# Performance work log

Hardware: AMD Instinct MI355X
Metric: run time of the kernel (lower is better)

The kernel has to match this reference:

```python
import jax, jax.numpy as jnp
import numpy as np

V, N, D, H, C = 3, 4096, 512, 128, 5  # views, nodes, in_dim, hidden, classes
NEG = -9.0e15   # mask value from original code (-9000000000000000.0)
NEG_SLOPE = 0.25


def _leaky(x, slope):
    return jnp.where(x >= 0, x, slope * x)


def setup_inputs() -> dict:
    key = jax.random.key(0)
    ks = jax.random.split(key, 24)
    g = lambda i, shape, s=0.05: (jax.random.normal(ks[i], shape, dtype=jnp.float32) * s)
    return {
        "data": jax.random.normal(ks[0], (V, N, D), dtype=jnp.float32),
        "adj": jax.random.randint(ks[1], (V, N, N), 0, 2, dtype=jnp.int32),
        "gac_w": g(2, (V, D, H)), "gac_b": g(3, (V, H)),
        "a1": g(4, (V, H)), "a2": g(5, (V, H)),
        "mlp_w": g(6, (V, D, H)), "mlp_b": g(7, (V, H)),
        "q_w": g(8, (V, H, H)), "q_b": g(9, (V, H)),
        "k_w": g(10, (V, H, H)), "k_b": g(11, (V, H)),
        "v_w": g(12, (V, H, H)), "v_b": g(13, (V, H)),
        "fc_w": g(14, (V, H, H)), "fc_b": g(15, (V, H)),
        "conf_w": g(16, (V, H, 1)), "conf_b": g(17, (V, 1)),
        "mm_w": g(18, (V * H, C)), "mm_b": g(19, (C,)),
    }


def reference(data, adj, gac_w, gac_b, a1, a2, mlp_w, mlp_b,
              q_w, q_b, k_w, k_b, v_w, v_b, fc_w, fc_b,
              conf_w, conf_b, mm_w, mm_b):
    # --- GraphAttentionConv (per view, vectorized over v) ---
    h = jnp.einsum('vnd,vdh->vnh', data, gac_w)               # spmm(input, W)
    e1 = jnp.einsum('vnh,vh->vn', h, a1)                      # h @ a1
    e2 = jnp.einsum('vnh,vh->vn', h, a2)                      # h @ a2
    e = _leaky(e1[:, :, None] + e2[:, None, :], NEG_SLOPE)    # [V,N,N] broadcast-add
    e = jnp.where(adj > 0, e, NEG)                            # mask by dense adjacency
    att = jax.nn.softmax(e, axis=-1)                          # row softmax
    feat = jnp.einsum('vnm,vmh->vnh', att, h) + gac_b[:, None, :]
    feat = _leaky(feat, NEG_SLOPE)                            # F.leaky_relu(GAC out, 0.25)
    # residual MLP branch
    feat = feat + jnp.einsum('vnd,vdh->vnh', data, mlp_w) + mlp_b[:, None, :]

    # --- StructureGuidedFeatureEnhancement (n_heads=1): per-node HxH attention ---
    Q = jnp.einsum('vnh,vho->vno', feat, q_w) + q_b[:, None, :]
    K = jnp.einsum('vnh,vho->vno', feat, k_w) + k_b[:, None, :]
    Vv = jnp.einsum('vnh,vho->vno', feat, v_w) + v_b[:, None, :]
    scale = jnp.sqrt(jnp.asarray(H, jnp.float32))
    A = Q[:, :, :, None] * K[:, :, None, :] / scale           # [V,N,H,H] outer product
    A = jax.nn.softmax(A, axis=-1)
    agg = jnp.einsum('vnio,vno->vni', A, Vv)                  # attention @ V
    agg = jnp.einsum('vnh,vho->vno', agg, fc_w) + fc_b[:, None, :]
    feat = jax.nn.relu(agg)

    # --- TCP confidence gating ---
    conf = jnp.einsum('vnh,vho->vno', feat, conf_w) + conf_b[:, None, :]  # [V,N,1]
    feat = feat * conf

    # --- concat views along feature dim, final classifier ---
    mm = jnp.transpose(feat, (1, 0, 2)).reshape(N, V * H)     # [N, V*H]
    return mm @ mm_w + mm_b                                   # MMlogit [N, C]
```

## Files before the change

kernel.cpp:

```cpp
#include <hip/hip_runtime.h>
#include <hip/hip_bf16.h>

#define V 3
#define N 4096
#define D 512
#define H 128
#define C 5
#define KS 4
#define M2 64
#define M1 32
#define LOG2E 1.4426950408889634f

typedef short short8 __attribute__((ext_vector_type(8)));
typedef float floatx4 __attribute__((ext_vector_type(4)));
typedef int   intx4  __attribute__((ext_vector_type(4)));

__device__ __forceinline__ unsigned short f2bf(float f){
  __hip_bfloat16 h = __float2bfloat16(f);
  return *reinterpret_cast<unsigned short*>(&h);
}
__device__ __forceinline__ unsigned int pk_bf16(float a, float b){
  unsigned int ua = __float_as_uint(a), ub = __float_as_uint(b);
  ua += 0x7FFFu + ((ua >> 16) & 1u);
  ub += 0x7FFFu + ((ub >> 16) & 1u);
  return (ua >> 16) | (ub & 0xFFFF0000u);
}

__global__ __launch_bounds__(256) void k0_wt(
    const float* __restrict__ gw, const float* __restrict__ mw,
    unsigned short* __restrict__ wT)
{
  const int v = blockIdx.x, m = blockIdx.y, kc = blockIdx.z;
  const int t = threadIdx.x;
  __shared__ unsigned short tr[128*72];
  const float* src = (m ? mw : gw) + (size_t)v*D*H + (size_t)kc*64*H;
  for (int i = t; i < 64*128; i += 256){
    int kk = i >> 7, col = i & 127;
    tr[col*72 + kk] = f2bf(src[i]);
  }
  __syncthreads();
  const int col = t >> 1, half = t & 1;
  uint4* dst = (uint4*)(wT + (((size_t)m*V + v)*H + col)*D + kc*64 + half*32);
  const unsigned short* s = &tr[col*72 + half*32];
  dst[0] = *(const uint4*)(s);
  dst[1] = *(const uint4*)(s + 8);
  dst[2] = *(const uint4*)(s + 16);
  dst[3] = *(const uint4*)(s + 24);
}

__global__ __launch_bounds__(256) void k0b_wt(
    const float* __restrict__ qw, const float* __restrict__ kw,
    const float* __restrict__ vw, const float* __restrict__ fw,
    unsigned short* __restrict__ wq4T)
{
  const int v = blockIdx.x, m = blockIdx.y, kc = blockIdx.z;
  const int t = threadIdx.x;
  __shared__ unsigned short tr[128*72];
  const float* src = (m==0?qw: m==1?kw: m==2?vw: fw) + (size_t)v*H*H + (size_t)kc*64*H;
  for (int i = t; i < 64*128; i += 256){
    int kk = i >> 7, col = i & 127;
    tr[col*72 + kk] = f2bf(src[i]);
  }
  __syncthreads();
  const int col = t >> 1, half = t & 1;
  uint4* dst = (uint4*)(wq4T + (((size_t)m*V + v)*H + col)*H + kc*64 + half*32);
  const unsigned short* s = &tr[col*72 + half*32];
  dst[0] = *(const uint4*)(s);
  dst[1] = *(const uint4*)(s + 8);
  dst[2] = *(const uint4*)(s + 16);
  dst[3] = *(const uint4*)(s + 24);
}

__global__ __launch_bounds__(512) void k1_gemm(
    const float* __restrict__ data, const unsigned short* __restrict__ wT,
    const float* __restrict__ a1, const float* __restrict__ a2,
    unsigned short* __restrict__ hT, float* __restrict__ mlp_out,
    float* __restrict__ e1g, float* __restrict__ e2g)
{
  const int v = blockIdx.y;
  const int n0 = blockIdx.x * M1;
  const int t = threadIdx.x;
  const int w = t >> 6, l = t & 63;
  __shared__ __align__(16) unsigned short AT[2][16][64][8];
  __shared__ float epart[2][M1][4];
  unsigned short* hTile = &AT[0][0][0][0];

  {
    const int r = t >> 4, oct = t & 15;
    const float4* dp = (const float4*)(data + ((size_t)v*N + n0 + r)*D + oct*32);
    float4 f[8];
    #pragma unroll
    for (int i=0;i<8;i++) f[i] = dp[i];
    #pragma unroll
    for (int q=0;q<4;q++){
      uint4 u;
      u.x = pk_bf16(f[2*q].x,   f[2*q].y);
      u.y = pk_bf16(f[2*q].z,   f[2*q].w);
      u.z = pk_bf16(f[2*q+1].x, f[2*q+1].y);
      u.w = pk_bf16(f[2*q+1].z, f[2*q+1].w);
      *(uint4*)&AT[r>>4][oct][(r&15) + 16*q][0] = u;
    }
  }
  __syncthreads();
  const int m = w >> 2, cb = (w & 3)*32;
  const int quad = l >> 4, c16 = l & 15;
  const unsigned short* b0 = wT + (((size_t)m*V + v)*H + cb + c16)*D + quad*8;
  floatx4 acc[2][2];
  #pragma unroll
  for (int rt=0;rt<2;rt++) for (int c=0;c<2;c++) acc[rt][c] = (floatx4){0.f,0.f,0.f,0.f};
  #pragma unroll
  for (int ks=0; ks<16; ks++){
    short8 a0 = *(const short8*)&AT[0][ks][l][0];
    short8 a1f = *(const short8*)&AT[1][ks][l][0];
    short8 bb0 = *(const short8*)(b0 + ks*32);
    short8 bb1 = *(const short8*)(b0 + 16*D + ks*32);
    acc[0][0] = __builtin_amdgcn_mfma_f32_16x16x32_bf16(a0,  bb0, acc[0][0], 0,0,0);
    acc[1][0] = __builtin_amdgcn_mfma_f32_16x16x32_bf16(a1f, bb0, acc[1][0], 0,0,0);
    acc[0][1] = __builtin_amdgcn_mfma_f32_16x16x32_bf16(a0,  bb1, acc[0][1], 0,0,0);
    acc[1][1] = __builtin_amdgcn_mfma_f32_16x16x32_bf16(a1f, bb1, acc[1][1], 0,0,0);
  }
  if (m == 1){
    #pragma unroll
    for (int rt=0;rt<2;rt++)
      #pragma unroll
      for (int c=0;c<2;c++)
        #pragma unroll
        for (int reg=0;reg<4;reg++){
          const int row = rt*16 + quad*4 + reg, col = cb + c*16 + c16;
          mlp_out[((size_t)v*N + n0 + row)*H + col] = acc[rt][c][reg];
        }
  } else {
    const float a1v0 = a1[v*H + cb + c16],      a2v0 = a2[v*H + cb + c16];
    const float a1v1 = a1[v*H + cb + 16 + c16], a2v1 = a2[v*H + cb + 16 + c16];
    #pragma unroll
    for (int rt=0;rt<2;rt++)
      #pragma unroll
      for (int reg=0;reg<4;reg++){
        float p1 = acc[rt][0][reg]*a1v0 + acc[rt][1][reg]*a1v1;
        float p2 = acc[rt][0][reg]*a2v0 + acc[rt][1][reg]*a2v1;
        p1 += __shfl_xor(p1,1); p1 += __shfl_xor(p1,2);
        p1 += __shfl_xor(p1,4); p1 += __shfl_xor(p1,8);
        p2 += __shfl_xor(p2,1); p2 += __shfl_xor(p2,2);
        p2 += __shfl_xor(p2,4); p2 += __shfl_xor(p2,8);
        if (c16 == 0){
          epart[0][rt*16 + quad*4 + reg][w] = p1;
          epart[1][rt*16 + quad*4 + reg][w] = p2;
        }
      }
  }
  __syncthreads();
  if (m == 0){
    #pragma unroll
    for (int rt=0;rt<2;rt++)
      #pragma unroll
      for (int c=0;c<2;c++)
        #pragma unroll
        for (int reg=0;reg<4;reg++){
          const int row = rt*16 + quad*4 + reg, col = cb + c*16 + c16;
          hTile[col*40 + row] = f2bf(acc[rt][c][reg]);
        }
  }
  __syncthreads();
  if (t < 128){
    const unsigned short* s = &hTile[t*40];
    uint4* dst = (uint4*)(hT + ((size_t)v*H + t)*N + n0);
    dst[0] = *(const uint4*)(s);
    dst[1] = *(const uint4*)(s + 8);
    dst[2] = *(const uint4*)(s + 16);
    dst[3] = *(const uint4*)(s + 24);
  } else if (t < 128 + M1){
    const int r = t - 128;
    e1g[(size_t)v*N + n0 + r] = LOG2E*(epart[0][r][0]+epart[0][r][1]+epart[0][r][2]+epart[0][r][3]);
  } else if (t < 128 + 2*M1){
    const int r = t - 128 - M1;
    e2g[(size_t)v*N + n0 + r] = LOG2E*(epart[1][r][0]+epart[1][r][1]+epart[1][r][2]+epart[1][r][3]);
  }
}

__global__ __launch_bounds__(512, 4) void k2_attn(
    const unsigned short* __restrict__ hT, const int* __restrict__ adj,
    const float* __restrict__ e1g, const float* __restrict__ e2g,
    float* __restrict__ pacc, float* __restrict__ pdenG)
{
  const int v = blockIdx.z;
  const int ksid = blockIdx.y;
  const int n0 = blockIdx.x * M2;
  const int kbase = ksid * (N/KS);
  const int t = threadIdx.x;
  const int w = t >> 6, l = t & 63;
  __shared__ __align__(16) unsigned short Afrag[2][4][4][64][8];
  __shared__ float pden_sh[M2][4];

  const int ksl  = w & 3;
  const int quad = l >> 4;
  const int rt0  = w >> 2;
  const int row0 = rt0*16 + (l & 15);
  const int row1 = row0 + 32;
  const int koff = ksl*32 + quad*8;
  const intx4* ap0 = (const intx4*)(adj + ((size_t)v*N + n0 + row0)*N + kbase + koff);
  const intx4* ap1 = (const intx4*)(adj + ((size_t)v*N + n0 + row1)*N + kbase + koff);
  const float4* ep = (const float4*)(e2g + (size_t)v*N + kbase + koff);
  const float e1r0 = e1g[(size_t)v*N + n0 + row0];
  const float e1r1 = e1g[(size_t)v*N + n0 + row1];
  float psum0 = 0.f, psum1 = 0.f;

  const int col = w*16 + (l & 15);
  const unsigned short* bcol = hT + ((size_t)v*H + col)*N + kbase + quad*8;
  floatx4 acc[4];
  #pragma unroll
  for (int rt=0;rt<4;rt++) acc[rt] = (floatx4){0.f,0.f,0.f,0.f};

  intx4  a00 = __builtin_nontemporal_load(ap0);
  intx4  a01 = __builtin_nontemporal_load(ap0 + 1);
  intx4  a10 = __builtin_nontemporal_load(ap1);
  intx4  a11 = __builtin_nontemporal_load(ap1 + 1);
  float4 ev0 = ep[0];
  float4 ev1 = ep[1];

  const int NCH = (N/KS)/128;
  #pragma unroll 1
  for (int c = 0; c < NCH; c++){
    const int buf = c & 1;
    {
      float ev[8] = {ev0.x,ev0.y,ev0.z,ev0.w, ev1.x,ev1.y,ev1.z,ev1.w};
      int   aa[8] = {a00.x,a00.y,a00.z,a00.w, a01.x,a01.y,a01.z,a01.w};
      int   bb[8] = {a10.x,a10.y,a10.z,a10.w, a11.x,a11.y,a11.z,a11.w};
      float wa[8], wb[8];
      #pragma unroll
      for (int j=0;j<8;j++){
        float ya = e1r0 + ev[j];
        ya = fmaxf(ya, 0.25f*ya);
        float ea = exp2f(ya);
        wa[j] = (aa[j] > 0) ? ea : 0.f;
        psum0 += wa[j];
        float yb = e1r1 + ev[j];
        yb = fmaxf(yb, 0.25f*yb);
        float eb = exp2f(yb);
        wb[j] = (bb[j] > 0) ? eb : 0.f;
        psum1 += wb[j];
      }
      union { short8 s; unsigned int u[4]; } pa, pb;
      #pragma unroll
      for (int j=0;j<4;j++){
        pa.u[j] = pk_bf16(wa[2*j], wa[2*j+1]);
        pb.u[j] = pk_bf16(wb[2*j], wb[2*j+1]);
      }
      *(short8*)&Afrag[buf][rt0  ][ksl][l][0] = pa.s;
      *(short8*)&Afrag[buf][rt0+2][ksl][l][0] = pb.s;
    }
    if (c+1 < NCH){
      a00 = __builtin_nontemporal_load(ap0 + (c+1)*32);
      a01 = __builtin_nontemporal_load(ap0 + (c+1)*32 + 1);
      a10 = __builtin_nontemporal_load(ap1 + (c+1)*32);
      a11 = __builtin_nontemporal_load(ap1 + (c+1)*32 + 1);
      ev0 = ep[(c+1)*32];
      ev1 = ep[(c+1)*32 + 1];
    }
    __syncthreads();
    #pragma unroll
    for (int ks=0; ks<4; ks++){
      short8 b8 = *(const short8*)(bcol + c*128 + ks*32);
      #pragma unroll
      for (int rt=0; rt<4; rt++){
        short8 a8 = *(const short8*)&Afrag[buf][rt][ks][l][0];
        acc[rt] = __builtin_amdgcn_mfma_f32_16x16x32_bf16(a8, b8, acc[rt], 0, 0, 0);
      }
    }
    __syncthreads();
  }
  psum0 += __shfl_xor(psum0, 16);
  psum0 += __shfl_xor(psum0, 32);
  psum1 += __shfl_xor(psum1, 16);
  psum1 += __shfl_xor(psum1, 32);
  if (l < 16){
    pden_sh[row0][ksl] = psum0;
    pden_sh[row1][ksl] = psum1;
  }
  __syncthreads();
  const size_t pb = ((size_t)v*KS + ksid)*(N/M2) + blockIdx.x;
  float* pa = pacc + pb*(M2*H);
  #pragma unroll
  for (int rt=0; rt<4; rt++){
    #pragma unroll
    for (int reg=0; reg<4; reg++){
      const int row = rt*16 + quad*4 + reg;
      pa[row*H + col] = acc[rt][reg];
    }
  }
  if (t < M2){
    float den = pden_sh[t][0] + pden_sh[t][1] + pden_sh[t][2] + pden_sh[t][3];
    pdenG[pb*M2 + t] = den;
  }
}

__global__ __launch_bounds__(256) void k3_sgfe(
    const float* __restrict__ pacc, const float* __restrict__ pdenG,
    const float* __restrict__ mlp_out,
    const float* __restrict__ gac_b, const float* __restrict__ mlp_b,
    const unsigned short* __restrict__ wq4T,
    const float* __restrict__ qb, const float* __restrict__ kb,
    const float* __restrict__ vb, const float* __restrict__ fcb,
    const float* __restrict__ confw, const float* __restrict__ confb,
    float* __restrict__ feat2)
{
  const int v = blockIdx.y;
  const int n0 = blockIdx.x * 16;
  const int t = threadIdx.x;
  const int w = t >> 6, l = t & 63;
  const int c16 = l & 15, quad = l >> 4;
  __shared__ __align__(16) unsigned short Ffrag[4][64][8];
  __shared__ __align__(16) unsigned short Gfrag[4][64][8];
  __shared__ float Qs[16][H];
  __shared__ float2 KVs[16][H];
  __shared__ float pc[16][4];
  __shared__ float confs[16];

  {
    const int col = t & 127, rh = t >> 7;
    const int bx2 = blockIdx.x >> 2;
    const int lr0 = (blockIdx.x & 3) * 16;
    const float gbv = gac_b[v*H + col];
    const float mbv = mlp_b[v*H + col];
    const int ks = col >> 5, q2 = (col & 31) >> 3, j = col & 7;
    #pragma unroll
    for (int i=0;i<8;i++){
      const int r = rh*8 + i;
      float num = 0.f, den = 0.f;
      #pragma unroll
      for (int s=0;s<KS;s++){
        const size_t pb = ((size_t)v*KS + s)*(N/M2) + bx2;
        num += pacc[pb*(M2*H) + (size_t)(lr0+r)*H + col];
        den += pdenG[pb*M2 + lr0 + r];
      }
      float x = num/den + gbv;
      x = (x >= 0.f) ? x : 0.25f*x;
      x += mlp_out[((size_t)v*N + n0 + r)*H + col] + mbv;
      Ffrag[ks][r + 16*q2][j] = f2bf(x);
    }
  }
  __syncthreads();
  const int colw0 = 2*w*16 + c16;
  {
    const unsigned short* bq = wq4T + (((size_t)0*V + v)*H + colw0)*H + quad*8;
    const unsigned short* bk = wq4T + (((size_t)1*V + v)*H + colw0)*H + quad*8;
    const unsigned short* bv = wq4T + (((size_t)2*V + v)*H + colw0)*H + quad*8;
    floatx4 aq[2], ak[2], av[2];
    #pragma unroll
    for (int c=0;c<2;c++){ aq[c]=(floatx4){0,0,0,0}; ak[c]=(floatx4){0,0,0,0}; av[c]=(floatx4){0,0,0,0}; }
    #pragma unroll
    for (int ks=0; ks<4; ks++){
      short8 a8 = *(const short8*)&Ffrag[ks][l][0];
      #pragma unroll
      for (int c=0;c<2;c++){
        short8 q8 = *(const short8*)(bq + (size_t)c*16*H + ks*32);
        short8 k8 = *(const short8*)(bk + (size_t)c*16*H + ks*32);
        short8 v8 = *(const short8*)(bv + (size_t)c*16*H + ks*32);
        aq[c] = __builtin_amdgcn_mfma_f32_16x16x32_bf16(a8, q8, aq[c], 0,0,0);
        ak[c] = __builtin_amdgcn_mfma_f32_16x16x32_bf16(a8, k8, ak[c], 0,0,0);
        av[c] = __builtin_amdgcn_mfma_f32_16x16x32_bf16(a8, v8, av[c], 0,0,0);
      }
    }
    #pragma unroll
    for (int c=0;c<2;c++){
      const int col = colw0 + c*16;
      const float qbv = qb[v*H+col], kbv = kb[v*H+col], vbv = vb[v*H+col];
      #pragma unroll
      for (int reg=0;reg<4;reg++){
        const int node = quad*4 + reg;
        Qs[node][col] = aq[c][reg] + qbv;
        KVs[node][col] = make_float2(ak[c][reg] + kbv, av[c][reg] + vbv);
      }
    }
  }
  __syncthreads();
  const float invs = 0.08838834764831845f;
  #pragma unroll
  for (int p=0;p<4;p++){
    const int r = 4*w + p;
    const float qa  = Qs[r][l]    * invs;
    const float qb2 = Qs[r][l+64] * invs;
    float sA=0.f, aA=0.f, sB=0.f, aB=0.f;
    const float4* kvp = (const float4*)&KVs[r][0];
    #pragma unroll 4
    for (int oo=0; oo<H/2; oo++){
      float4 kv2 = kvp[oo];
      float eA0 = __expf(qa*kv2.x);  sA += eA0; aA = fmaf(eA0, kv2.y, aA);
      float eA1 = __expf(qa*kv2.z);  sA += eA1; aA = fmaf(eA1, kv2.w, aA);
      float eB0 = __expf(qb2*kv2.x); sB += eB0; aB = fmaf(eB0, kv2.y, aB);
      float eB1 = __expf(qb2*kv2.z); sB += eB1; aB = fmaf(eB1, kv2.w, aB);
    }
    Gfrag[l>>5][r + 16*((l&31)>>3)][l&7] = f2bf(aA/sA);
    Gfrag[2 + (l>>5)][r + 16*((l&31)>>3)][l&7] = f2bf(aB/sB);
  }
  __syncthreads();
  const unsigned short* bf = wq4T + (((size_t)3*V + v)*H + colw0)*H + quad*8;
  floatx4 af[2];
  af[0]=(floatx4){0,0,0,0}; af[1]=(floatx4){0,0,0,0};
  #pragma unroll
  for (int ks=0; ks<4; ks++){
    short8 a8 = *(const short8*)&Gfrag[ks][l][0];
    #pragma unroll
    for (int c=0;c<2;c++){
      short8 b8 = *(const short8*)(bf + (size_t)c*16*H + ks*32);
      af[c] = __builtin_amdgcn_mfma_f32_16x16x32_bf16(a8, b8, af[c], 0,0,0);
    }
  }
  float g[2][4];
  float pn[4] = {0.f,0.f,0.f,0.f};
  #pragma unroll
  for (int c=0;c<2;c++){
    const int col = colw0 + c*16;
    const float fcbv = fcb[v*H+col];
    const float cwv  = confw[v*H+col];
    #pragma unroll
    for (int reg=0;reg<4;reg++){
      float gg = fmaxf(af[c][reg] + fcbv, 0.f);
      g[c][reg] = gg;
      pn[reg] += gg*cwv;
    }
  }
  #pragma unroll
  for (int reg=0;reg<4;reg++){
    pn[reg] += __shfl_xor(pn[reg], 1);
    pn[reg] += __shfl_xor(pn[reg], 2);
    pn[reg] += __shfl_xor(pn[reg], 4);
    pn[reg] += __shfl_xor(pn[reg], 8);
  }
  if (c16 == 0){
    #pragma unroll
    for (int reg=0;reg<4;reg++) pc[quad*4 + reg][w] = pn[reg];
  }
  __syncthreads();
  if (t < 16) confs[t] = pc[t][0] + pc[t][1] + pc[t][2] + pc[t][3] + confb[v];
  __syncthreads();
  #pragma unroll
  for (int c=0;c<2;c++){
    const int col = colw0 + c*16;
    #pragma unroll
    for (int reg=0;reg<4;reg++){
      const int node = quad*4 + reg;
      feat2[((size_t)v*N + n0 + node)*H + col] = g[c][reg]*confs[node];
    }
  }
}

__global__ __launch_bounds__(64) void k4_cls(
    const float* __restrict__ feat2,
    const float* __restrict__ mm_w, const float* __restrict__ mm_b,
    float* __restrict__ out)
{
  const int n = blockIdx.x, t = threadIdx.x;
  float a[C] = {0,0,0,0,0};
  for (int j=t; j<V*H; j+=64){
    int vv = j >> 7, hh = j & (H-1);
    float f = feat2[((size_t)vv*N + n)*H + hh];
    #pragma unroll
    for (int c=0;c<C;c++) a[c] = fmaf(f, mm_w[j*C+c], a[c]);
  }
  #pragma unroll
  for (int c=0;c<C;c++){
    #pragma unroll
    for (int o=32;o>0;o>>=1) a[c] += __shfl_down(a[c],o);
  }
  if (t==0){
    #pragma unroll
    for (int c=0;c<C;c++) out[(size_t)n*C+c] = a[c] + mm_b[c];
  }
}

extern "C" void kernel_launch(void* const* d_in, const int* in_sizes, int n_in,
                              void* d_out, int out_size, void* d_ws, size_t ws_size,
                              hipStream_t stream)
{
  (void)in_sizes; (void)n_in; (void)out_size; (void)ws_size;
  const float* data  = (const float*)d_in[0];
  const int*   adj   = (const int*)d_in[1];
  const float* gac_w = (const float*)d_in[2];
  const float* gac_b = (const float*)d_in[3];
  const float* a1    = (const float*)d_in[4];
  const float* a2    = (const float*)d_in[5];
  const float* mlp_w = (const float*)d_in[6];
  const float* mlp_b = (const float*)d_in[7];
  const float* q_w   = (const float*)d_in[8];
  const float* q_b   = (const float*)d_in[9];
  const float* k_w   = (const float*)d_in[10];
  const float* k_b   = (const float*)d_in[11];
  const float* v_w   = (const float*)d_in[12];
  const float* v_b   = (const float*)d_in[13];
  const float* fc_w  = (const float*)d_in[14];
  const float* fc_b  = (const float*)d_in[15];
  const float* cw    = (const float*)d_in[16];
  const float* cb    = (const float*)d_in[17];
  const float* mm_w  = (const float*)d_in[18];
  const float* mm_b  = (const float*)d_in[19];

  float* ws = (float*)d_ws;
  const size_t VNH = (size_t)V*N*H;
  float* mlp   = ws;
  float* feat2 = ws + VNH;
  float* e1    = ws + 2*VNH;
  float* e2    = e1 + (size_t)V*N;
  unsigned short* hT   = (unsigned short*)(e2 + (size_t)V*N);
  unsigned short* wT   = hT + VNH;
  unsigned short* wq4T = wT + (size_t)2*V*H*D;
  float* pacc  = (float*)(wq4T + (size_t)4*V*H*H);
  float* pden  = pacc + (size_t)V*KS*(N/M2)*M2*H;

  k0_wt  <<<dim3(V, 2, D/64), 256, 0, stream>>>(gac_w, mlp_w, wT);
  k0b_wt <<<dim3(V, 4, H/64), 256, 0, stream>>>(q_w, k_w, v_w, fc_w, wq4T);
  k1_gemm<<<dim3(N/M1, V),    512, 0, stream>>>(data, wT, a1, a2, hT, mlp, e1, e2);
  k2_attn<<<dim3(N/M2, KS, V),512, 0, stream>>>(hT, adj, e1, e2, pacc, pden);
  k3_sgfe<<<dim3(N/16, V),    256, 0, stream>>>(pacc, pden, mlp, gac_b, mlp_b,
                                                wq4T, q_b, k_b, v_b, fc_b,
                                                cw, cb, feat2);
  k4_cls <<<dim3(N),           64, 0, stream>>>(feat2, mm_w, mm_b, (float*)d_out);
}
```

Baseline: 428.5 us.

## Merge weight-prep kernels, halve attention split-K, fold softmax scale into exp2

Merges the two weight-transpose kernels into a single launch of 72 blocks. Halves the split-K factor of the graph-attention kernel, which cuts partial-sum traffic and reduction work in the next kernel but gives fewer blocks to run in parallel. Pre-multiplies Q by scale*log2e so the inner exponentials use exp2f. Packs four nodes per classifier block so fewer, larger blocks are launched.

```diff
diff --git a/kernel.cpp b/kernel.cpp
--- a/kernel.cpp
+++ b/kernel.cpp
@@ -6,7 +6,7 @@
 #define D 512
 #define H 128
 #define C 5
-#define KS 4
+#define KS 2
 #define M2 64
 #define M1 32
 #define LOG2E 1.4426950408889634f
@@ -26,44 +26,35 @@
   return (ua >> 16) | (ub & 0xFFFF0000u);
 }
 
-__global__ __launch_bounds__(256) void k0_wt(
+__global__ __launch_bounds__(256) void k0_all(
     const float* __restrict__ gw, const float* __restrict__ mw,
-    unsigned short* __restrict__ wT)
+    const float* __restrict__ qw, const float* __restrict__ kw,
+    const float* __restrict__ vw, const float* __restrict__ fw,
+    unsigned short* __restrict__ wT, unsigned short* __restrict__ wq4T)
 {
-  const int v = blockIdx.x, m = blockIdx.y, kc = blockIdx.z;
-  const int t = threadIdx.x;
+  const int b = blockIdx.x, t = threadIdx.x;
   __shared__ unsigned short tr[128*72];
-  const float* src = (m ? mw : gw) + (size_t)v*D*H + (size_t)kc*64*H;
+  const float* src;
+  unsigned short* dst0;
+  int K, koff;
+  if (b < 48){
+    const int v = b % V, r = b / V, m = r & 1, kc = r >> 1;
+    src  = (m ? mw : gw) + (size_t)v*D*H + (size_t)kc*64*H;
+    dst0 = wT + ((size_t)m*V + v)*(size_t)H*D;
+    K = D; koff = kc*64;
+  } else {
+    const int j = b - 48, v = j % V, r = j / V, m = r & 3, kc = r >> 2;
+    src  = (m==0?qw: m==1?kw: m==2?vw: fw) + (size_t)v*H*H + (size_t)kc*64*H;
+    dst0 = wq4T + ((size_t)m*V + v)*(size_t)H*H;
+    K = H; koff = kc*64;
+  }
   for (int i = t; i < 64*128; i += 256){
     int kk = i >> 7, col = i & 127;
     tr[col*72 + kk] = f2bf(src[i]);
   }
   __syncthreads();
   const int col = t >> 1, half = t & 1;
-  uint4* dst = (uint4*)(wT + (((size_t)m*V + v)*H + col)*D + kc*64 + half*32);
-  const unsigned short* s = &tr[col*72 + half*32];
-  dst[0] = *(const uint4*)(s);
-  dst[1] = *(const uint4*)(s + 8);
-  dst[2] = *(const uint4*)(s + 16);
-  dst[3] = *(const uint4*)(s + 24);
-}
-
-__global__ __launch_bounds__(256) void k0b_wt(
-    const float* __restrict__ qw, const float* __restrict__ kw,
-    const float* __restrict__ vw, const float* __restrict__ fw,
-    unsigned short* __restrict__ wq4T)
-{
-  const int v = blockIdx.x, m = blockIdx.y, kc = blockIdx.z;
-  const int t = threadIdx.x;
-  __shared__ unsigned short tr[128*72];
-  const float* src = (m==0?qw: m==1?kw: m==2?vw: fw) + (size_t)v*H*H + (size_t)kc*64*H;
-  for (int i = t; i < 64*128; i += 256){
-    int kk = i >> 7, col = i & 127;
-    tr[col*72 + kk] = f2bf(src[i]);
-  }
-  __syncthreads();
-  const int col = t >> 1, half = t & 1;
-  uint4* dst = (uint4*)(wq4T + (((size_t)m*V + v)*H + col)*H + kc*64 + half*32);
+  uint4* dst = (uint4*)(dst0 + (size_t)col*K + koff + half*32);
   const unsigned short* s = &tr[col*72 + half*32];
   dst[0] = *(const uint4*)(s);
   dst[1] = *(const uint4*)(s + 8);
@@ -340,6 +331,7 @@
   }
   __syncthreads();
   const int colw0 = 2*w*16 + c16;
+  const float QSC = 0.08838834764831845f * LOG2E;
   {
     const unsigned short* bq = wq4T + (((size_t)0*V + v)*H + colw0)*H + quad*8;
     const unsigned short* bk = wq4T + (((size_t)1*V + v)*H + colw0)*H + quad*8;
@@ -367,27 +359,26 @@
       #pragma unroll
       for (int reg=0;reg<4;reg++){
         const int node = quad*4 + reg;
-        Qs[node][col] = aq[c][reg] + qbv;
+        Qs[node][col] = (aq[c][reg] + qbv) * QSC;
         KVs[node][col] = make_float2(ak[c][reg] + kbv, av[c][reg] + vbv);
       }
     }
   }
   __syncthreads();
-  const float invs = 0.08838834764831845f;
   #pragma unroll
   for (int p=0;p<4;p++){
     const int r = 4*w + p;
-    const float qa  = Qs[r][l]    * invs;
-    const float qb2 = Qs[r][l+64] * invs;
+    const float qa  = Qs[r][l];
+    const float qb2 = Qs[r][l+64];
     float sA=0.f, aA=0.f, sB=0.f, aB=0.f;
     const float4* kvp = (const float4*)&KVs[r][0];
     #pragma unroll 4
     for (int oo=0; oo<H/2; oo++){
       float4 kv2 = kvp[oo];
-      float eA0 = __expf(qa*kv2.x);  sA += eA0; aA = fmaf(eA0, kv2.y, aA);
-      float eA1 = __expf(qa*kv2.z);  sA += eA1; aA = fmaf(eA1, kv2.w, aA);
-      float eB0 = __expf(qb2*kv2.x); sB += eB0; aB = fmaf(eB0, kv2.y, aB);
-      float eB1 = __expf(qb2*kv2.z); sB += eB1; aB = fmaf(eB1, kv2.w, aB);
+      float eA0 = exp2f(qa*kv2.x);  sA += eA0; aA = fmaf(eA0, kv2.y, aA);
+      float eA1 = exp2f(qa*kv2.z);  sA += eA1; aA = fmaf(eA1, kv2.w, aA);
+      float eB0 = exp2f(qb2*kv2.x); sB += eB0; aB = fmaf(eB0, kv2.y, aB);
+      float eB1 = exp2f(qb2*kv2.z); sB += eB1; aB = fmaf(eB1, kv2.w, aB);
     }
     Gfrag[l>>5][r + 16*((l&31)>>3)][l&7] = f2bf(aA/sA);
     Gfrag[2 + (l>>5)][r + 16*((l&31)>>3)][l&7] = f2bf(aB/sB);
@@ -444,12 +435,13 @@
   }
 }
 
-__global__ __launch_bounds__(64) void k4_cls(
+__global__ __launch_bounds__(256) void k4_cls(
     const float* __restrict__ feat2,
     const float* __restrict__ mm_w, const float* __restrict__ mm_b,
     float* __restrict__ out)
 {
-  const int n = blockIdx.x, t = threadIdx.x;
+  const int n = blockIdx.x*4 + (threadIdx.x >> 6);
+  const int t = threadIdx.x & 63;
   float a[C] = {0,0,0,0,0};
   for (int j=t; j<V*H; j+=64){
     int vv = j >> 7, hh = j & (H-1);
@@ -506,12 +498,11 @@
   float* pacc  = (float*)(wq4T + (size_t)4*V*H*H);
   float* pden  = pacc + (size_t)V*KS*(N/M2)*M2*H;
 
-  k0_wt  <<<dim3(V, 2, D/64), 256, 0, stream>>>(gac_w, mlp_w, wT);
-  k0b_wt <<<dim3(V, 4, H/64), 256, 0, stream>>>(q_w, k_w, v_w, fc_w, wq4T);
-  k1_gemm<<<dim3(N/M1, V),    512, 0, stream>>>(data, wT, a1, a2, hT, mlp, e1, e2);
-  k2_attn<<<dim3(N/M2, KS, V),512, 0, stream>>>(hT, adj, e1, e2, pacc, pden);
-  k3_sgfe<<<dim3(N/16, V),    256, 0, stream>>>(pacc, pden, mlp, gac_b, mlp_b,
-                                                wq4T, q_b, k_b, v_b, fc_b,
-                                                cw, cb, feat2);
-  k4_cls <<<dim3(N),           64, 0, stream>>>(feat2, mm_w, mm_b, (float*)d_out);
-}
+  k0_all <<<dim3(72),          256, 0, stream>>>(gac_w, mlp_w, q_w, k_w, v_w, fc_w, wT, wq4T);
+  k1_gemm<<<dim3(N/M1, V),     512, 0, stream>>>(data, wT, a1, a2, hT, mlp, e1, e2);
+  k2_attn<<<dim3(N/M2, KS, V), 512, 0, stream>>>(hT, adj, e1, e2, pacc, pden);
+  k3_sgfe<<<dim3(N/16, V),     256, 0, stream>>>(pacc, pden, mlp, gac_b, mlp_b,
+                                                 wq4T, q_b, k_b, v_b, fc_b,
+                                                 cw, cb, feat2);
+  k4_cls <<<dim3(N/4),         256, 0, stream>>>(feat2, mm_w, mm_b, (float*)d_out);
+}
```

Result: slower. 440.9 us (+2.9%).
